# Kernel optimization log

Hardware: AMD Instinct MI355X
Metric: run time of the kernel (lower is better)

The kernel has to match this reference:

```python
import jax, jax.numpy as jnp
import numpy as np


def setup_inputs() -> dict:
    key = jax.random.key(0)
    ks = jax.random.split(key, 7)
    T, B, D, H, Q = 256, 128, 1024, 2048, 1024
    return {
        "x": jax.random.normal(ks[0], (T, B, D), dtype=jnp.float32),
        "h0": jax.random.normal(ks[1], (B, H), dtype=jnp.float32) * 0.01,
        "W_xh": jax.random.normal(ks[2], (D, H), dtype=jnp.float32) * 0.01,
        "W_hh": jax.random.normal(ks[3], (H, H), dtype=jnp.float32) * 0.01,
        "b_h": jnp.zeros((H,), dtype=jnp.float32),
        "W_hq": jax.random.normal(ks[4], (H, Q), dtype=jnp.float32) * 0.01,
        "b_q": jnp.zeros((Q,), dtype=jnp.float32),
    }


def reference(x, h0, W_xh, W_hh, b_h, W_hq, b_q):
    # x: (T, B, D); vanilla RNN recurrence with ReLU, per-step output projection.
    def step(h, xt):
        h = jax.nn.relu(xt @ W_xh + h @ W_hh + b_h)  # (B, H)
        return h, h @ W_hq + b_q                      # (B, Q)

    h, outs = jax.lax.scan(step, h0, x)               # outs: (T, B, Q)
    out = outs.reshape(-1, outs.shape[-1])            # torch.cat along dim 0 -> (T*B, Q)
    return out, h
```

## Files before the change

kernel.cpp:

```cpp
#include <hip/hip_runtime.h>
#include <hip/hip_bf16.h>

typedef __bf16 bf16_t;
typedef bf16_t bf16x8 __attribute__((ext_vector_type(8)));
typedef bf16_t bf16x4 __attribute__((ext_vector_type(4)));
typedef bf16_t bf16x2 __attribute__((ext_vector_type(2)));
typedef float f32x4 __attribute__((ext_vector_type(4)));
typedef float f32x2 __attribute__((ext_vector_type(2)));

__device__ __forceinline__ void load_lds16(const bf16_t* g, bf16_t* l) {
  __builtin_amdgcn_global_load_lds(
      (const __attribute__((address_space(1))) unsigned int*)g,
      (__attribute__((address_space(3))) unsigned int*)l,
      16, 0, 0);
}

__global__ void conv_f32_bf16(const float* __restrict__ src,
                              bf16_t* __restrict__ dst, long n) {
  long i = ((long)blockIdx.x * blockDim.x + threadIdx.x) * 8;
  if (i + 7 >= n) return;
  float4 a = *(const float4*)(src + i);
  float4 b = *(const float4*)(src + i + 4);
  bf16x8 v;
  v[0] = (bf16_t)a.x; v[1] = (bf16_t)a.y; v[2] = (bf16_t)a.z; v[3] = (bf16_t)a.w;
  v[4] = (bf16_t)b.x; v[5] = (bf16_t)b.y; v[6] = (bf16_t)b.z; v[7] = (bf16_t)b.w;
  *(bf16x8*)(dst + i) = v;
}

__global__ void conv_bf16_f32(const bf16_t* __restrict__ src,
                              float* __restrict__ dst, long n) {
  long i = (long)blockIdx.x * blockDim.x + threadIdx.x;
  if (i >= n) return;
  dst[i] = (float)src[i];
}

__global__ void transpose_conv(const float* __restrict__ src,
                               bf16_t* __restrict__ dst, int Ksrc, int Nsrc) {
  __shared__ float tile[32][33];
  int n0 = blockIdx.x * 32, k0 = blockIdx.y * 32;
  int tx = threadIdx.x, ty = threadIdx.y;
#pragma unroll
  for (int i = 0; i < 32; i += 8)
    tile[ty + i][tx] = src[(long)(k0 + ty + i) * Nsrc + n0 + tx];
  __syncthreads();
#pragma unroll
  for (int i = 0; i < 32; i += 8)
    dst[(long)(n0 + ty + i) * Ksrc + k0 + tx] = (bf16_t)tile[tx][ty + i];
}

template <int STORE_MODE>
__global__ __launch_bounds__(256) void gemm_bt_128(
    const bf16_t* __restrict__ A, const bf16_t* __restrict__ Bt,
    const float* __restrict__ bias, void* __restrict__ Dout,
    int M, int N, int K) {
  __shared__ bf16_t As[128 * 32];
  __shared__ bf16_t Bs[128 * 32];
  const int tid = threadIdx.x;
  const int lane = tid & 63;
  const int w = tid >> 6;
  const int wr = w >> 1, wc = w & 1;
  const int m0 = blockIdx.y * 128, n0 = blockIdx.x * 128;

  f32x4 acc[4][4] = {};

  const int r0 = tid >> 2;
  const int kk = (tid & 3) * 8;
  const int fr = lane & 15;
  const int fk = (lane >> 4) * 8;

  for (int k0 = 0; k0 < K; k0 += 32) {
    load_lds16(A + (long)(m0 + r0) * K + k0 + kk, As + w * 512);
    load_lds16(A + (long)(m0 + 64 + r0) * K + k0 + kk, As + 2048 + w * 512);
    load_lds16(Bt + (long)(n0 + r0) * K + k0 + kk, Bs + w * 512);
    load_lds16(Bt + (long)(n0 + 64 + r0) * K + k0 + kk, Bs + 2048 + w * 512);
    asm volatile("s_waitcnt vmcnt(0)" ::: "memory");
    __syncthreads();

    bf16x8 af[4], bfx[4];
#pragma unroll
    for (int m = 0; m < 4; ++m)
      af[m] = *(const bf16x8*)&As[(wr * 64 + m * 16 + fr) * 32 + fk];
#pragma unroll
    for (int n = 0; n < 4; ++n)
      bfx[n] = *(const bf16x8*)&Bs[(wc * 64 + n * 16 + fr) * 32 + fk];
#pragma unroll
    for (int m = 0; m < 4; ++m)
#pragma unroll
      for (int n = 0; n < 4; ++n)
        acc[m][n] = __builtin_amdgcn_mfma_f32_16x16x32_bf16(af[m], bfx[n],
                                                            acc[m][n], 0, 0, 0);
    __syncthreads();
  }

  const int fq = lane >> 4;
#pragma unroll
  for (int m = 0; m < 4; ++m) {
#pragma unroll
    for (int n = 0; n < 4; ++n) {
      int col = n0 + wc * 64 + n * 16 + fr;
      float bv = bias[col];
#pragma unroll
      for (int r = 0; r < 4; ++r) {
        int row = m0 + wr * 64 + m * 16 + fq * 4 + r;
        float v = acc[m][n][r] + bv;
        if (STORE_MODE == 0)
          ((float*)Dout)[(long)row * N + col] = v;
        else
          ((bf16_t*)Dout)[(long)row * N + col] = (bf16_t)v;
      }
    }
  }
}

__device__ __forceinline__ void half_bar(unsigned int* c, unsigned int target,
                                         int lane) {
  if (lane == 0)
    __hip_atomic_fetch_add(c, 1u, __ATOMIC_RELEASE,
                           __HIP_MEMORY_SCOPE_WORKGROUP);
  unsigned int v;
  do {
    v = __hip_atomic_load(c, __ATOMIC_ACQUIRE, __HIP_MEMORY_SCOPE_WORKGROUP);
    if (v >= target) break;
    __builtin_amdgcn_s_sleep(1);
  } while (true);
}

__global__ __launch_bounds__(512, 1) void rnn_persistent14(
    const bf16_t* __restrict__ h0,
    bf16_t* __restrict__ Hbuf,
    const bf16_t* __restrict__ WhhT,
    const bf16_t* __restrict__ WhqT,
    const float* __restrict__ bq,
    float* __restrict__ out,
    unsigned int* __restrict__ flags) {
  __shared__ bf16_t Wlds[65536];
  __shared__ float sred[2][4][16 * 36];
  __shared__ bf16_t qred[2][4][16 * 20];
  __shared__ unsigned int barc[2];
  __shared__ unsigned int sfree[2];
  __shared__ unsigned int qbc[2];
  __shared__ unsigned int qfree[2];

  const int tid = threadIdx.x, lane = tid & 63, w = tid >> 6;
  const int h = w >> 2;
  const int lw = w & 3;
  const int gid = blockIdx.x;
  const int p = (gid >> 1) & 3;
  const int n0idx = ((gid & 1) << 5) | (gid >> 3);
  const int chain = p + h * 4;
  const int m0 = chain * 16, n0 = n0idx * 32;
  const int H = 2048;
  const long BH = 128L * 2048;
  const int kb = lw * 512;
  const int fr = lane & 15, fg = lane >> 4;
  const int w64 = lw * 64;
  const int qcol0 = n0idx * 16;

  {
    const int scol = tid >> 4;
    const int sk16 = tid & 15;
    const bf16_t* gsrc = WhhT + (long)(n0 + scol) * H + sk16 * 8;
#pragma unroll 4
    for (int j = 0; j < 16; ++j) {
      bf16x8 v = *(const bf16x8*)(gsrc + j * 128);
      int k8 = sk16 + j * 16;
      *(bf16x8*)&Wlds[(k8 * 32 + scol) * 8] = v;
    }
  }
  if (tid < 2) { barc[tid] = 0; sfree[tid] = 0; qbc[tid] = 0; qfree[tid] = 0; }

  const bf16_t* Wq = WhqT + (long)(qcol0 + fr) * H + kb + fg * 8;
#define LOADPIN(dst, off)                                                     \
  bf16x8 dst = *(const bf16x8*)(Wq + (off));                                  \
  {                                                                           \
    f32x4 t_ = __builtin_bit_cast(f32x4, dst);                                \
    asm volatile("" : "+v"(t_));                                              \
    dst = __builtin_bit_cast(bf16x8, t_);                                     \
  }
  LOADPIN(q0, 0)    LOADPIN(q1, 32)   LOADPIN(q2, 64)   LOADPIN(q3, 96)
  LOADPIN(q4, 128)  LOADPIN(q5, 160)  LOADPIN(q6, 192)  LOADPIN(q7, 224)
  LOADPIN(q8, 256)  LOADPIN(q9, 288)  LOADPIN(q10, 320) LOADPIN(q11, 352)
  LOADPIN(q12, 384) LOADPIN(q13, 416) LOADPIN(q14, 448) LOADPIN(q15, 480)
#undef LOADPIN
  __syncthreads();

  if (h == 1) __builtin_amdgcn_s_sleep(64);

  const int zrowW = lane >> 2, zcolW = (lane & 3) * 8;
  const int sidx = zrowW * 36 + zcolW;
  const long zoffW = (long)(m0 + zrowW) * H + n0 + zcolW;

  const int qrow = lane >> 2, qc4 = (lane & 3) * 4;
  const f32x4 bqv = *(const f32x4*)(bq + qcol0 + qc4);

  unsigned int* myflag = flags + (((chain << 6) | n0idx) << 4);
  const unsigned int* pollflag =
      flags + (((chain << 6) | (lw * 16 + (lane & 15))) << 4);
  unsigned int* bc = &barc[h];
  unsigned int* sf = &sfree[h];
  unsigned int* qc = &qbc[h];
  unsigned int* qf = &qfree[h];

  for (int t = 0; t < 256; ++t) {
    const bf16_t* hp = (t == 0) ? h0 : Hbuf + (long)(t - 1) * BH;
    bf16_t* z = Hbuf + (long)t * BH;
    const int ew = t & 3;
    const int ew2 = (t + 2) & 3;

    f32x4 zvr;
    if (lw == ew) {
      const bf16_t* zp = z + zoffW;
      asm volatile("global_load_dwordx4 %0, %1, off sc0 sc1"
                   : "=v"(zvr)
                   : "v"(zp)
                   : "memory");
    }

    if (t > 0) {
      const unsigned int tt = (unsigned int)t;
      unsigned int v = __hip_atomic_load(pollflag, __ATOMIC_RELAXED,
                                         __HIP_MEMORY_SCOPE_AGENT);
      if (!__all(v >= tt)) {
        __builtin_amdgcn_s_sleep(1);
        v = __hip_atomic_load(pollflag, __ATOMIC_RELAXED,
                              __HIP_MEMORY_SCOPE_AGENT);
        if (!__all(v >= tt)) {
          __builtin_amdgcn_s_sleep(2);
          v = __hip_atomic_load(pollflag, __ATOMIC_RELAXED,
                                __HIP_MEMORY_SCOPE_AGENT);
          if (!__all(v >= tt)) {
            __builtin_amdgcn_s_sleep(4);
            v = __hip_atomic_load(pollflag, __ATOMIC_RELAXED,
                                  __HIP_MEMORY_SCOPE_AGENT);
            while (!__all(v >= tt)) {
              __builtin_amdgcn_s_sleep(8);
              v = __hip_atomic_load(pollflag, __ATOMIC_RELAXED,
                                    __HIP_MEMORY_SCOPE_AGENT);
            }
          }
        }
      }
    }

    const bf16_t* Ab = hp + (long)(m0 + fr) * H + kb + fg * 8;
    f32x4 a0, a1, a2, a3, a4, a5, a6, a7, a8, a9, a10, a11, a12, a13, a14, a15;
    asm volatile(
        "global_load_dwordx4 %0, %16, off sc0\n\t"
        "global_load_dwordx4 %1, %16, off offset:64 sc0\n\t"
        "global_load_dwordx4 %2, %16, off offset:128 sc0\n\t"
        "global_load_dwordx4 %3, %16, off offset:192 sc0\n\t"
        "global_load_dwordx4 %4, %16, off offset:256 sc0\n\t"
        "global_load_dwordx4 %5, %16, off offset:320 sc0\n\t"
        "global_load_dwordx4 %6, %16, off offset:384 sc0\n\t"
        "global_load_dwordx4 %7, %16, off offset:448 sc0\n\t"
        "global_load_dwordx4 %8, %16, off offset:512 sc0\n\t"
        "global_load_dwordx4 %9, %16, off offset:576 sc0\n\t"
        "global_load_dwordx4 %10, %16, off offset:640 sc0\n\t"
        "global_load_dwordx4 %11, %16, off offset:704 sc0\n\t"
        "global_load_dwordx4 %12, %16, off offset:768 sc0\n\t"
        "global_load_dwordx4 %13, %16, off offset:832 sc0\n\t"
        "global_load_dwordx4 %14, %16, off offset:896 sc0\n\t"
        "global_load_dwordx4 %15, %16, off offset:960 sc0"
        : "=&v"(a0), "=&v"(a1), "=&v"(a2), "=&v"(a3), "=&v"(a4), "=&v"(a5),
          "=&v"(a6), "=&v"(a7), "=&v"(a8), "=&v"(a9), "=&v"(a10), "=&v"(a11),
          "=&v"(a12), "=&v"(a13), "=&v"(a14), "=&v"(a15)
        : "v"(Ab)
        : "memory");

    f32x4 acc0 = {}, acc1 = {};
#define STEPX(ks, A)                                                          \
  {                                                                           \
    bf16x8 w0 = *(const bf16x8*)&Wlds[((w64 + (ks) * 4 + fg) * 32 + fr) * 8]; \
    bf16x8 w1 =                                                               \
        *(const bf16x8*)&Wlds[((w64 + (ks) * 4 + fg) * 32 + 16 + fr) * 8];    \
    bf16x8 av = __builtin_bit_cast(bf16x8, A);                                \
    acc0 = __builtin_amdgcn_mfma_f32_16x16x32_bf16(av, w0, acc0, 0, 0, 0);    \
    acc1 = __builtin_amdgcn_mfma_f32_16x16x32_bf16(av, w1, acc1, 0, 0, 0);    \
  }
    asm volatile("s_waitcnt vmcnt(8)" ::: "memory");
    __builtin_amdgcn_sched_barrier(0);
    STEPX(0, a0)   STEPX(1, a1)   STEPX(2, a2)   STEPX(3, a3)
    STEPX(4, a4)   STEPX(5, a5)   STEPX(6, a6)   STEPX(7, a7)
    asm volatile("s_waitcnt vmcnt(0)" ::: "memory");
    __builtin_amdgcn_sched_barrier(0);
    STEPX(8, a8)   STEPX(9, a9)   STEPX(10, a10) STEPX(11, a11)
    STEPX(12, a12) STEPX(13, a13) STEPX(14, a14) STEPX(15, a15)
#undef STEPX

    if (t > 0) {
      while (__hip_atomic_load(sf, __ATOMIC_ACQUIRE,
                               __HIP_MEMORY_SCOPE_WORKGROUP) <
             (unsigned int)t)
        __builtin_amdgcn_s_sleep(1);
    }

#pragma unroll
    for (int rr = 0; rr < 4; ++rr) {
      sred[h][lw][(fg * 4 + rr) * 36 + fr] = acc0[rr];
      sred[h][lw][(fg * 4 + rr) * 36 + 16 + fr] = acc1[rr];
    }
    half_bar(bc, (unsigned int)(t + 1) * 4, lane);

    if (lw == ew) {
      f32x4 slo = *(const f32x4*)&sred[h][0][sidx];
      f32x4 shi = *(const f32x4*)&sred[h][0][sidx + 4];
#pragma unroll
      for (int ww = 1; ww < 4; ++ww) {
        slo = slo + *(const f32x4*)&sred[h][ww][sidx];
        shi = shi + *(const f32x4*)&sred[h][ww][sidx + 4];
      }
      bf16x8 zv = __builtin_bit_cast(bf16x8, zvr);
      bf16x8 o;
#pragma unroll
      for (int c = 0; c < 4; ++c) {
        float v0 = slo[c] + (float)zv[c];
        float v1 = shi[c] + (float)zv[c + 4];
        o[c] = (bf16_t)(v0 > 0.f ? v0 : 0.f);
        o[c + 4] = (bf16_t)(v1 > 0.f ? v1 : 0.f);
      }
      const bf16_t* zp = z + zoffW;
      {
        f32x4 ov = __builtin_bit_cast(f32x4, o);
        asm volatile("global_store_dwordx4 %0, %1, off sc0 sc1" ::"v"(zp),
                     "v"(ov)
                     : "memory");
      }
      asm volatile("s_waitcnt vmcnt(0)" ::: "memory");
      if (lane == 0) {
        __hip_atomic_store(myflag, (unsigned int)(t + 1), __ATOMIC_RELAXED,
                           __HIP_MEMORY_SCOPE_AGENT);
        __hip_atomic_store(sf, (unsigned int)(t + 1), __ATOMIC_RELEASE,
                           __HIP_MEMORY_SCOPE_WORKGROUP);
      }
    }

    if (t > 0) {
      f32x4 qacc = {};
#define QSTEP(A, QW)                                                          \
  qacc = __builtin_amdgcn_mfma_f32_16x16x32_bf16(                             \
      __builtin_bit_cast(bf16x8, A), QW, qacc, 0, 0, 0);
      QSTEP(a0, q0)   QSTEP(a1, q1)   QSTEP(a2, q2)   QSTEP(a3, q3)
      QSTEP(a4, q4)   QSTEP(a5, q5)   QSTEP(a6, q6)   QSTEP(a7, q7)
      QSTEP(a8, q8)   QSTEP(a9, q9)   QSTEP(a10, q10) QSTEP(a11, q11)
      QSTEP(a12, q12) QSTEP(a13, q13) QSTEP(a14, q14) QSTEP(a15, q15)
#undef QSTEP
      while (__hip_atomic_load(qf, __ATOMIC_ACQUIRE,
                               __HIP_MEMORY_SCOPE_WORKGROUP) <
             (unsigned int)(t - 1))
        __builtin_amdgcn_s_sleep(1);
#pragma unroll
      for (int rr = 0; rr < 4; ++rr)
        qred[h][lw][(fg * 4 + rr) * 20 + fr] = (bf16_t)qacc[rr];
      half_bar(qc, (unsigned int)t * 4, lane);

      if (lw == ew2) {
        f32x4 s = bqv;
#pragma unroll
        for (int ww = 0; ww < 4; ++ww)
#pragma unroll
          for (int j = 0; j < 4; ++j)
            s[j] += (float)qred[h][ww][qrow * 20 + qc4 + j];
        float* op = out + ((long)(t - 1) * 128 + m0 + qrow) * 1024 + qcol0 + qc4;
        *(f32x4*)op = s;
        if (lane == 0)
          __hip_atomic_store(qf, (unsigned int)t, __ATOMIC_RELEASE,
                             __HIP_MEMORY_SCOPE_WORKGROUP);
      }
    }
  }

  {
    const unsigned int tt = 256u;
    unsigned int v;
    do {
      v = __hip_atomic_load(pollflag, __ATOMIC_RELAXED,
                            __HIP_MEMORY_SCOPE_AGENT);
      if (__all(v >= tt)) break;
      __builtin_amdgcn_s_sleep(2);
    } while (true);

    const bf16_t* hp = Hbuf + 255L * BH;
    const bf16_t* Ab = hp + (long)(m0 + fr) * H + kb + fg * 8;
    f32x4 a0, a1, a2, a3, a4, a5, a6, a7, a8, a9, a10, a11, a12, a13, a14, a15;
    asm volatile(
        "global_load_dwordx4 %0, %16, off sc0\n\t"
        "global_load_dwordx4 %1, %16, off offset:64 sc0\n\t"
        "global_load_dwordx4 %2, %16, off offset:128 sc0\n\t"
        "global_load_dwordx4 %3, %16, off offset:192 sc0\n\t"
        "global_load_dwordx4 %4, %16, off offset:256 sc0\n\t"
        "global_load_dwordx4 %5, %16, off offset:320 sc0\n\t"
        "global_load_dwordx4 %6, %16, off offset:384 sc0\n\t"
        "global_load_dwordx4 %7, %16, off offset:448 sc0\n\t"
        "global_load_dwordx4 %8, %16, off offset:512 sc0\n\t"
        "global_load_dwordx4 %9, %16, off offset:576 sc0\n\t"
        "global_load_dwordx4 %10, %16, off offset:640 sc0\n\t"
        "global_load_dwordx4 %11, %16, off offset:704 sc0\n\t"
        "global_load_dwordx4 %12, %16, off offset:768 sc0\n\t"
        "global_load_dwordx4 %13, %16, off offset:832 sc0\n\t"
        "global_load_dwordx4 %14, %16, off offset:896 sc0\n\t"
        "global_load_dwordx4 %15, %16, off offset:960 sc0\n\t"
        "s_waitcnt vmcnt(0)"
        : "=&v"(a0), "=&v"(a1), "=&v"(a2), "=&v"(a3), "=&v"(a4), "=&v"(a5),
          "=&v"(a6), "=&v"(a7), "=&v"(a8), "=&v"(a9), "=&v"(a10), "=&v"(a11),
          "=&v"(a12), "=&v"(a13), "=&v"(a14), "=&v"(a15)
        : "v"(Ab)
        : "memory");
    __builtin_amdgcn_sched_barrier(0);

    f32x4 qacc = {};
#define QSTEP(A, QW)                                                          \
  qacc = __builtin_amdgcn_mfma_f32_16x16x32_bf16(                             \
      __builtin_bit_cast(bf16x8, A), QW, qacc, 0, 0, 0);
    QSTEP(a0, q0)   QSTEP(a1, q1)   QSTEP(a2, q2)   QSTEP(a3, q3)
    QSTEP(a4, q4)   QSTEP(a5, q5)   QSTEP(a6, q6)   QSTEP(a7, q7)
    QSTEP(a8, q8)   QSTEP(a9, q9)   QSTEP(a10, q10) QSTEP(a11, q11)
    QSTEP(a12, q12) QSTEP(a13, q13) QSTEP(a14, q14) QSTEP(a15, q15)
#undef QSTEP
    while (__hip_atomic_load(qf, __ATOMIC_ACQUIRE,
                             __HIP_MEMORY_SCOPE_WORKGROUP) < 255u)
      __builtin_amdgcn_s_sleep(1);
#pragma unroll
    for (int rr = 0; rr < 4; ++rr)
      qred[h][lw][(fg * 4 + rr) * 20 + fr] = (bf16_t)qacc[rr];
    half_bar(qc, 256u * 4, lane);

    if (lw == ((256 + 2) & 3)) {
      f32x4 s = bqv;
#pragma unroll
      for (int ww = 0; ww < 4; ++ww)
#pragma unroll
        for (int j = 0; j < 4; ++j)
          s[j] += (float)qred[h][ww][qrow * 20 + qc4 + j];
      float* op = out + (255L * 128 + m0 + qrow) * 1024 + qcol0 + qc4;
      *(f32x4*)op = s;
    }
  }
}

extern "C" void kernel_launch(void* const* d_in, const int* in_sizes, int n_in,
                              void* d_out, int out_size, void* d_ws,
                              size_t ws_size, hipStream_t stream) {
  const float* x   = (const float*)d_in[0];
  const float* h0  = (const float*)d_in[1];
  const float* Wxh = (const float*)d_in[2];
  const float* Whh = (const float*)d_in[3];
  const float* bh  = (const float*)d_in[4];
  const float* Whq = (const float*)d_in[5];
  const float* bq  = (const float*)d_in[6];
  float* out = (float*)d_out;

  const int T = 256, B = 128, D = 1024, H = 2048, Q = 1024;
  const long MB = (long)T * B;

  char* ws = (char*)d_ws;
  unsigned int* flags = (unsigned int*)ws;  ws += 512 * 64;
  bf16_t* x_bf = (bf16_t*)ws;  ws += MB * D * 2;
  bf16_t* Hbuf = (bf16_t*)ws;  ws += MB * H * 2;
  bf16_t* h0bf = (bf16_t*)ws;  ws += (long)B * H * 2;
  bf16_t* WxhT = (bf16_t*)ws;  ws += (long)H * D * 2;
  bf16_t* WhhT = (bf16_t*)ws;  ws += (long)H * H * 2;
  bf16_t* WhqT = (bf16_t*)ws;  ws += (long)Q * H * 2;

  hipMemsetAsync(flags, 0, 512 * 64, stream);

  conv_f32_bf16<<<(int)(MB * D / 8 / 256), 256, 0, stream>>>(x, x_bf, MB * D);
  conv_f32_bf16<<<(int)((long)B * H / 8 / 256), 256, 0, stream>>>(h0, h0bf,
                                                                  (long)B * H);
  transpose_conv<<<dim3(H / 32, D / 32), dim3(32, 8), 0, stream>>>(Wxh, WxhT, D, H);
  transpose_conv<<<dim3(H / 32, H / 32), dim3(32, 8), 0, stream>>>(Whh, WhhT, H, H);
  transpose_conv<<<dim3(Q / 32, H / 32), dim3(32, 8), 0, stream>>>(Whq, WhqT, H, Q);

  gemm_bt_128<1><<<dim3(H / 128, MB / 128), 256, 0, stream>>>(
      x_bf, WxhT, bh, Hbuf, (int)MB, H, D);

  rnn_persistent14<<<256, 512, 0, stream>>>(h0bf, Hbuf, WhhT, WhqT, bq, out,
                                            flags);

  conv_bf16_f32<<<(int)((long)B * H / 256), 256, 0, stream>>>(
      Hbuf + (long)(T - 1) * B * H, out + MB * Q, (long)B * H);
}
```

Before: 1.564 ms.

## Fuse input projection GEMM into persistent RNN kernel with register-pinned W_xh slices

Removes the separate x@W_xh GEMM kernel and computes each step's input projection inside the persistent recurrence kernel. Each wave pins its slice of W_xh in registers, loads the x tile for the step, and runs the MFMAs before the h@W_hh part; the bias is now added in the epilogue. This eliminates a large prepass GEMM and the bf16 Hbuf round-trip of the projected input. In exchange it adds per-step global loads and MFMA work, plus extra register pressure, inside the latency-critical serial loop.

Measured after the change: 1.621 ms. +3.6%, slower.

```diff
diff --git a/kernel.cpp b/kernel.cpp
--- a/kernel.cpp
+++ b/kernel.cpp
@@ -4,7 +4,6 @@
 typedef __bf16 bf16_t;
 typedef bf16_t bf16x8 __attribute__((ext_vector_type(8)));
 typedef bf16_t bf16x4 __attribute__((ext_vector_type(4)));
-typedef bf16_t bf16x2 __attribute__((ext_vector_type(2)));
 typedef float f32x4 __attribute__((ext_vector_type(4)));
 typedef float f32x2 __attribute__((ext_vector_type(2)));
 
@@ -46,70 +45,6 @@
 #pragma unroll
   for (int i = 0; i < 32; i += 8)
     dst[(long)(n0 + ty + i) * Ksrc + k0 + tx] = (bf16_t)tile[tx][ty + i];
-}
-
-template <int STORE_MODE>
-__global__ __launch_bounds__(256) void gemm_bt_128(
-    const bf16_t* __restrict__ A, const bf16_t* __restrict__ Bt,
-    const float* __restrict__ bias, void* __restrict__ Dout,
-    int M, int N, int K) {
-  __shared__ bf16_t As[128 * 32];
-  __shared__ bf16_t Bs[128 * 32];
-  const int tid = threadIdx.x;
-  const int lane = tid & 63;
-  const int w = tid >> 6;
-  const int wr = w >> 1, wc = w & 1;
-  const int m0 = blockIdx.y * 128, n0 = blockIdx.x * 128;
-
-  f32x4 acc[4][4] = {};
-
-  const int r0 = tid >> 2;
-  const int kk = (tid & 3) * 8;
-  const int fr = lane & 15;
-  const int fk = (lane >> 4) * 8;
-
-  for (int k0 = 0; k0 < K; k0 += 32) {
-    load_lds16(A + (long)(m0 + r0) * K + k0 + kk, As + w * 512);
-    load_lds16(A + (long)(m0 + 64 + r0) * K + k0 + kk, As + 2048 + w * 512);
-    load_lds16(Bt + (long)(n0 + r0) * K + k0 + kk, Bs + w * 512);
-    load_lds16(Bt + (long)(n0 + 64 + r0) * K + k0 + kk, Bs + 2048 + w * 512);
-    asm volatile("s_waitcnt vmcnt(0)" ::: "memory");
-    __syncthreads();
-
-    bf16x8 af[4], bfx[4];
-#pragma unroll
-    for (int m = 0; m < 4; ++m)
-      af[m] = *(const bf16x8*)&As[(wr * 64 + m * 16 + fr) * 32 + fk];
-#pragma unroll
-    for (int n = 0; n < 4; ++n)
-      bfx[n] = *(const bf16x8*)&Bs[(wc * 64 + n * 16 + fr) * 32 + fk];
-#pragma unroll
-    for (int m = 0; m < 4; ++m)
-#pragma unroll
-      for (int n = 0; n < 4; ++n)
-        acc[m][n] = __builtin_amdgcn_mfma_f32_16x16x32_bf16(af[m], bfx[n],
-                                                            acc[m][n], 0, 0, 0);
-    __syncthreads();
-  }
-
-  const int fq = lane >> 4;
-#pragma unroll
-  for (int m = 0; m < 4; ++m) {
-#pragma unroll
-    for (int n = 0; n < 4; ++n) {
-      int col = n0 + wc * 64 + n * 16 + fr;
-      float bv = bias[col];
-#pragma unroll
-      for (int r = 0; r < 4; ++r) {
-        int row = m0 + wr * 64 + m * 16 + fq * 4 + r;
-        float v = acc[m][n][r] + bv;
-        if (STORE_MODE == 0)
-          ((float*)Dout)[(long)row * N + col] = v;
-        else
-          ((bf16_t*)Dout)[(long)row * N + col] = (bf16_t)v;
-      }
-    }
-  }
 }
 
 __device__ __forceinline__ void half_bar(unsigned int* c, unsigned int target,
@@ -125,10 +60,13 @@
   } while (true);
 }
 
-__global__ __launch_bounds__(512, 1) void rnn_persistent14(
+__global__ __launch_bounds__(512, 1) void rnn_persistent15(
     const bf16_t* __restrict__ h0,
+    const bf16_t* __restrict__ xb,
     bf16_t* __restrict__ Hbuf,
     const bf16_t* __restrict__ WhhT,
+    const bf16_t* __restrict__ WxhT,
+    const float* __restrict__ bh,
     const bf16_t* __restrict__ WhqT,
     const float* __restrict__ bq,
     float* __restrict__ out,
@@ -152,6 +90,7 @@
   const int H = 2048;
   const long BH = 128L * 2048;
   const int kb = lw * 512;
+  const int kbx = lw * 256;
   const int fr = lane & 15, fg = lane >> 4;
   const int w64 = lw * 64;
   const int qcol0 = n0idx * 16;
@@ -169,18 +108,28 @@
   }
   if (tid < 2) { barc[tid] = 0; sfree[tid] = 0; qbc[tid] = 0; qfree[tid] = 0; }
 
-  const bf16_t* Wq = WhqT + (long)(qcol0 + fr) * H + kb + fg * 8;
-#define LOADPIN(dst, off)                                                     \
-  bf16x8 dst = *(const bf16x8*)(Wq + (off));                                  \
+#define LOADPIN(dst, addr)                                                    \
+  bf16x8 dst = *(const bf16x8*)(addr);                                        \
   {                                                                           \
     f32x4 t_ = __builtin_bit_cast(f32x4, dst);                                \
     asm volatile("" : "+v"(t_));                                              \
     dst = __builtin_bit_cast(bf16x8, t_);                                     \
   }
-  LOADPIN(q0, 0)    LOADPIN(q1, 32)   LOADPIN(q2, 64)   LOADPIN(q3, 96)
-  LOADPIN(q4, 128)  LOADPIN(q5, 160)  LOADPIN(q6, 192)  LOADPIN(q7, 224)
-  LOADPIN(q8, 256)  LOADPIN(q9, 288)  LOADPIN(q10, 320) LOADPIN(q11, 352)
-  LOADPIN(q12, 384) LOADPIN(q13, 416) LOADPIN(q14, 448) LOADPIN(q15, 480)
+  const bf16_t* Wq = WhqT + (long)(qcol0 + fr) * H + kb + fg * 8;
+  LOADPIN(q0, Wq + 0)    LOADPIN(q1, Wq + 32)   LOADPIN(q2, Wq + 64)
+  LOADPIN(q3, Wq + 96)   LOADPIN(q4, Wq + 128)  LOADPIN(q5, Wq + 160)
+  LOADPIN(q6, Wq + 192)  LOADPIN(q7, Wq + 224)  LOADPIN(q8, Wq + 256)
+  LOADPIN(q9, Wq + 288)  LOADPIN(q10, Wq + 320) LOADPIN(q11, Wq + 352)
+  LOADPIN(q12, Wq + 384) LOADPIN(q13, Wq + 416) LOADPIN(q14, Wq + 448)
+  LOADPIN(q15, Wq + 480)
+  const bf16_t* Wx0 = WxhT + (long)(n0 + fr) * 1024 + kbx + fg * 8;
+  const bf16_t* Wx1 = WxhT + (long)(n0 + 16 + fr) * 1024 + kbx + fg * 8;
+  LOADPIN(wx0, Wx0 + 0)   LOADPIN(wx1, Wx0 + 32)  LOADPIN(wx2, Wx0 + 64)
+  LOADPIN(wx3, Wx0 + 96)  LOADPIN(wx4, Wx0 + 128) LOADPIN(wx5, Wx0 + 160)
+  LOADPIN(wx6, Wx0 + 192) LOADPIN(wx7, Wx0 + 224)
+  LOADPIN(wy0, Wx1 + 0)   LOADPIN(wy1, Wx1 + 32)  LOADPIN(wy2, Wx1 + 64)
+  LOADPIN(wy3, Wx1 + 96)  LOADPIN(wy4, Wx1 + 128) LOADPIN(wy5, Wx1 + 160)
+  LOADPIN(wy6, Wx1 + 192) LOADPIN(wy7, Wx1 + 224)
 #undef LOADPIN
   __syncthreads();
 
@@ -189,6 +138,8 @@
   const int zrowW = lane >> 2, zcolW = (lane & 3) * 8;
   const int sidx = zrowW * 36 + zcolW;
   const long zoffW = (long)(m0 + zrowW) * H + n0 + zcolW;
+  const f32x4 bhlo = *(const f32x4*)(bh + n0 + zcolW);
+  const f32x4 bhhi = *(const f32x4*)(bh + n0 + zcolW + 4);
 
   const int qrow = lane >> 2, qc4 = (lane & 3) * 4;
   const f32x4 bqv = *(const f32x4*)(bq + qcol0 + qc4);
@@ -207,14 +158,21 @@
     const int ew = t & 3;
     const int ew2 = (t + 2) & 3;
 
-    f32x4 zvr;
-    if (lw == ew) {
-      const bf16_t* zp = z + zoffW;
-      asm volatile("global_load_dwordx4 %0, %1, off sc0 sc1"
-                   : "=v"(zvr)
-                   : "v"(zp)
-                   : "memory");
-    }
+    const bf16_t* Xb = xb + ((long)t * 128 + m0 + fr) * 1024 + kbx + fg * 8;
+    f32x4 x0, x1, x2, x3, x4, x5, x6, x7;
+    asm volatile(
+        "global_load_dwordx4 %0, %8, off sc0\n\t"
+        "global_load_dwordx4 %1, %8, off offset:64 sc0\n\t"
+        "global_load_dwordx4 %2, %8, off offset:128 sc0\n\t"
+        "global_load_dwordx4 %3, %8, off offset:192 sc0\n\t"
+        "global_load_dwordx4 %4, %8, off offset:256 sc0\n\t"
+        "global_load_dwordx4 %5, %8, off offset:320 sc0\n\t"
+        "global_load_dwordx4 %6, %8, off offset:384 sc0\n\t"
+        "global_load_dwordx4 %7, %8, off offset:448 sc0"
+        : "=&v"(x0), "=&v"(x1), "=&v"(x2), "=&v"(x3), "=&v"(x4), "=&v"(x5),
+          "=&v"(x6), "=&v"(x7)
+        : "v"(Xb)
+        : "memory");
 
     if (t > 0) {
       const unsigned int tt = (unsigned int)t;
@@ -241,6 +199,20 @@
         }
       }
     }
+
+    asm volatile("s_waitcnt vmcnt(0)" ::: "memory");
+    __builtin_amdgcn_sched_barrier(0);
+    f32x4 acc0 = {}, acc1 = {};
+#define XSTEP(A, W0, W1)                                                      \
+  {                                                                           \
+    bf16x8 av = __builtin_bit_cast(bf16x8, A);                                \
+    acc0 = __builtin_amdgcn_mfma_f32_16x16x32_bf16(av, W0, acc0, 0, 0, 0);    \
+    acc1 = __builtin_amdgcn_mfma_f32_16x16x32_bf16(av, W1, acc1, 0, 0, 0);    \
+  }
+    XSTEP(x0, wx0, wy0) XSTEP(x1, wx1, wy1) XSTEP(x2, wx2, wy2)
+    XSTEP(x3, wx3, wy3) XSTEP(x4, wx4, wy4) XSTEP(x5, wx5, wy5)
+    XSTEP(x6, wx6, wy6) XSTEP(x7, wx7, wy7)
+#undef XSTEP
 
     const bf16_t* Ab = hp + (long)(m0 + fr) * H + kb + fg * 8;
     f32x4 a0, a1, a2, a3, a4, a5, a6, a7, a8, a9, a10, a11, a12, a13, a14, a15;
@@ -267,7 +239,6 @@
         : "v"(Ab)
         : "memory");
 
-    f32x4 acc0 = {}, acc1 = {};
 #define STEPX(ks, A)                                                          \
   {                                                                           \
     bf16x8 w0 = *(const bf16x8*)&Wlds[((w64 + (ks) * 4 + fg) * 32 + fr) * 8]; \
@@ -309,12 +280,11 @@
         slo = slo + *(const f32x4*)&sred[h][ww][sidx];
         shi = shi + *(const f32x4*)&sred[h][ww][sidx + 4];
       }
-      bf16x8 zv = __builtin_bit_cast(bf16x8, zvr);
       bf16x8 o;
 #pragma unroll
       for (int c = 0; c < 4; ++c) {
-        float v0 = slo[c] + (float)zv[c];
-        float v1 = shi[c] + (float)zv[c + 4];
+        float v0 = slo[c] + bhlo[c];
+        float v1 = shi[c] + bhhi[c];
         o[c] = (bf16_t)(v0 > 0.f ? v0 : 0.f);
         o[c + 4] = (bf16_t)(v1 > 0.f ? v1 : 0.f);
       }
@@ -470,11 +440,8 @@
   transpose_conv<<<dim3(H / 32, H / 32), dim3(32, 8), 0, stream>>>(Whh, WhhT, H, H);
   transpose_conv<<<dim3(Q / 32, H / 32), dim3(32, 8), 0, stream>>>(Whq, WhqT, H, Q);
 
-  gemm_bt_128<1><<<dim3(H / 128, MB / 128), 256, 0, stream>>>(
-      x_bf, WxhT, bh, Hbuf, (int)MB, H, D);
-
-  rnn_persistent14<<<256, 512, 0, stream>>>(h0bf, Hbuf, WhhT, WhqT, bq, out,
-                                            flags);
+  rnn_persistent15<<<256, 512, 0, stream>>>(h0bf, x_bf, Hbuf, WhhT, WxhT, bh,
+                                            WhqT, bq, out, flags);
 
   conv_bf16_f32<<<(int)((long)B * H / 256), 256, 0, stream>>>(
       Hbuf + (long)(T - 1) * B * H, out + MB * Q, (long)B * H);
```

## Replace per-step flag handshakes with data-embedded sign-bit validity in double-buffered hidden slots

Applied to the files above, without the earlier changes.

Drops the global flag array and its store-wait-then-flag publish. Each step's hidden state now goes into one of two ping-pong slots, with the bf16 sign bits XOR-flipped on alternating slot generations, so consumers poll the data itself. A load counts as valid when every sign bit matches the expected parity, which works because ReLU outputs are non-negative. This removes a release round trip and a separate flag poll from the serial critical path, at the cost of re-reading the full A blob on every spin and an extra XOR decode. It also relies on bf16 stores of 16 bytes never being observed torn.

Result: slower. 1.893 ms (+21.0%).

```diff
diff --git a/kernel.cpp b/kernel.cpp
--- a/kernel.cpp
+++ b/kernel.cpp
@@ -3,10 +3,8 @@
 
 typedef __bf16 bf16_t;
 typedef bf16_t bf16x8 __attribute__((ext_vector_type(8)));
-typedef bf16_t bf16x4 __attribute__((ext_vector_type(4)));
-typedef bf16_t bf16x2 __attribute__((ext_vector_type(2)));
 typedef float f32x4 __attribute__((ext_vector_type(4)));
-typedef float f32x2 __attribute__((ext_vector_type(2)));
+typedef unsigned int u32x4 __attribute__((ext_vector_type(4)));
 
 __device__ __forceinline__ void load_lds16(const bf16_t* g, bf16_t* l) {
   __builtin_amdgcn_global_load_lds(
@@ -27,11 +25,12 @@
   *(bf16x8*)(dst + i) = v;
 }
 
-__global__ void conv_bf16_f32(const bf16_t* __restrict__ src,
-                              float* __restrict__ dst, long n) {
+__global__ void conv_dec_f32(const unsigned short* __restrict__ src,
+                             float* __restrict__ dst, long n) {
   long i = (long)blockIdx.x * blockDim.x + threadIdx.x;
   if (i >= n) return;
-  dst[i] = (float)src[i];
+  unsigned int u = ((unsigned int)(src[i] ^ 0x8000u)) << 16;
+  dst[i] = __builtin_bit_cast(float, u);
 }
 
 __global__ void transpose_conv(const float* __restrict__ src,
@@ -125,14 +124,39 @@
   } while (true);
 }
 
-__global__ __launch_bounds__(512, 1) void rnn_persistent14(
+#define ABLOB(P)                                                              \
+  asm volatile(                                                               \
+      "global_load_dwordx4 %0, %16, off sc0 sc1\n\t"                          \
+      "global_load_dwordx4 %1, %16, off offset:64 sc0 sc1\n\t"                \
+      "global_load_dwordx4 %2, %16, off offset:128 sc0 sc1\n\t"               \
+      "global_load_dwordx4 %3, %16, off offset:192 sc0 sc1\n\t"               \
+      "global_load_dwordx4 %4, %16, off offset:256 sc0 sc1\n\t"               \
+      "global_load_dwordx4 %5, %16, off offset:320 sc0 sc1\n\t"               \
+      "global_load_dwordx4 %6, %16, off offset:384 sc0 sc1\n\t"               \
+      "global_load_dwordx4 %7, %16, off offset:448 sc0 sc1\n\t"               \
+      "global_load_dwordx4 %8, %16, off offset:512 sc0 sc1\n\t"               \
+      "global_load_dwordx4 %9, %16, off offset:576 sc0 sc1\n\t"               \
+      "global_load_dwordx4 %10, %16, off offset:640 sc0 sc1\n\t"              \
+      "global_load_dwordx4 %11, %16, off offset:704 sc0 sc1\n\t"              \
+      "global_load_dwordx4 %12, %16, off offset:768 sc0 sc1\n\t"              \
+      "global_load_dwordx4 %13, %16, off offset:832 sc0 sc1\n\t"              \
+      "global_load_dwordx4 %14, %16, off offset:896 sc0 sc1\n\t"              \
+      "global_load_dwordx4 %15, %16, off offset:960 sc0 sc1\n\t"              \
+      "s_waitcnt vmcnt(0)"                                                    \
+      : "=&v"(a0), "=&v"(a1), "=&v"(a2), "=&v"(a3), "=&v"(a4), "=&v"(a5),     \
+        "=&v"(a6), "=&v"(a7), "=&v"(a8), "=&v"(a9), "=&v"(a10), "=&v"(a11),   \
+        "=&v"(a12), "=&v"(a13), "=&v"(a14), "=&v"(a15)                        \
+      : "v"(P)                                                                \
+      : "memory")
+
+__global__ __launch_bounds__(512, 1) void rnn_persistent17(
     const bf16_t* __restrict__ h0,
-    bf16_t* __restrict__ Hbuf,
+    const bf16_t* __restrict__ Zbuf,
+    bf16_t* __restrict__ Hslots,
     const bf16_t* __restrict__ WhhT,
     const bf16_t* __restrict__ WhqT,
     const float* __restrict__ bq,
-    float* __restrict__ out,
-    unsigned int* __restrict__ flags) {
+    float* __restrict__ out) {
   __shared__ bf16_t Wlds[65536];
   __shared__ float sred[2][4][16 * 36];
   __shared__ bf16_t qred[2][4][16 * 20];
@@ -193,79 +217,70 @@
   const int qrow = lane >> 2, qc4 = (lane & 3) * 4;
   const f32x4 bqv = *(const f32x4*)(bq + qcol0 + qc4);
 
-  unsigned int* myflag = flags + (((chain << 6) | n0idx) << 4);
-  const unsigned int* pollflag =
-      flags + (((chain << 6) | (lw * 16 + (lane & 15))) << 4);
   unsigned int* bc = &barc[h];
   unsigned int* sf = &sfree[h];
   unsigned int* qc = &qbc[h];
   unsigned int* qf = &qfree[h];
 
+  const long aoff = (long)(m0 + fr) * H + kb + fg * 8;
+
   for (int t = 0; t < 256; ++t) {
-    const bf16_t* hp = (t == 0) ? h0 : Hbuf + (long)(t - 1) * BH;
-    bf16_t* z = Hbuf + (long)t * BH;
+    const bf16_t* z = Zbuf + (long)t * BH;
     const int ew = t & 3;
     const int ew2 = (t + 2) & 3;
 
-    f32x4 zvr;
-    if (lw == ew) {
-      const bf16_t* zp = z + zoffW;
-      asm volatile("global_load_dwordx4 %0, %1, off sc0 sc1"
-                   : "=v"(zvr)
-                   : "v"(zp)
-                   : "memory");
-    }
-
-    if (t > 0) {
-      const unsigned int tt = (unsigned int)t;
-      unsigned int v = __hip_atomic_load(pollflag, __ATOMIC_RELAXED,
-                                         __HIP_MEMORY_SCOPE_AGENT);
-      if (!__all(v >= tt)) {
-        __builtin_amdgcn_s_sleep(1);
-        v = __hip_atomic_load(pollflag, __ATOMIC_RELAXED,
-                              __HIP_MEMORY_SCOPE_AGENT);
-        if (!__all(v >= tt)) {
-          __builtin_amdgcn_s_sleep(2);
-          v = __hip_atomic_load(pollflag, __ATOMIC_RELAXED,
-                                __HIP_MEMORY_SCOPE_AGENT);
-          if (!__all(v >= tt)) {
-            __builtin_amdgcn_s_sleep(4);
-            v = __hip_atomic_load(pollflag, __ATOMIC_RELAXED,
-                                  __HIP_MEMORY_SCOPE_AGENT);
-            while (!__all(v >= tt)) {
-              __builtin_amdgcn_s_sleep(8);
-              v = __hip_atomic_load(pollflag, __ATOMIC_RELAXED,
-                                    __HIP_MEMORY_SCOPE_AGENT);
-            }
-          }
+    f32x4 zvr = {};
+    if (lw == ew) zvr = *(const f32x4*)(z + zoffW);
+
+    f32x4 a0, a1, a2, a3, a4, a5, a6, a7, a8, a9, a10, a11, a12, a13, a14, a15;
+    if (t == 0) {
+      const bf16_t* Ab = h0 + aoff;
+      ABLOB(Ab);
+      __builtin_amdgcn_sched_barrier(0);
+    } else {
+      const bf16_t* Ab = Hslots + ((long)((t - 1) & 1)) * BH + aoff;
+      const unsigned int expect =
+          (((t - 1) >> 1) & 1) ? 0x80008000u : 0u;
+      for (;;) {
+        ABLOB(Ab);
+        __builtin_amdgcn_sched_barrier(0);
+        bool rdy;
+        if (expect) {
+          u32x4 m = __builtin_bit_cast(u32x4, a0);
+          m &= __builtin_bit_cast(u32x4, a1);  m &= __builtin_bit_cast(u32x4, a2);
+          m &= __builtin_bit_cast(u32x4, a3);  m &= __builtin_bit_cast(u32x4, a4);
+          m &= __builtin_bit_cast(u32x4, a5);  m &= __builtin_bit_cast(u32x4, a6);
+          m &= __builtin_bit_cast(u32x4, a7);  m &= __builtin_bit_cast(u32x4, a8);
+          m &= __builtin_bit_cast(u32x4, a9);  m &= __builtin_bit_cast(u32x4, a10);
+          m &= __builtin_bit_cast(u32x4, a11); m &= __builtin_bit_cast(u32x4, a12);
+          m &= __builtin_bit_cast(u32x4, a13); m &= __builtin_bit_cast(u32x4, a14);
+          m &= __builtin_bit_cast(u32x4, a15);
+          unsigned int c = m[0] & m[1] & m[2] & m[3];
+          rdy = ((~c) & 0x80008000u) == 0u;
+        } else {
+          u32x4 m = __builtin_bit_cast(u32x4, a0);
+          m |= __builtin_bit_cast(u32x4, a1);  m |= __builtin_bit_cast(u32x4, a2);
+          m |= __builtin_bit_cast(u32x4, a3);  m |= __builtin_bit_cast(u32x4, a4);
+          m |= __builtin_bit_cast(u32x4, a5);  m |= __builtin_bit_cast(u32x4, a6);
+          m |= __builtin_bit_cast(u32x4, a7);  m |= __builtin_bit_cast(u32x4, a8);
+          m |= __builtin_bit_cast(u32x4, a9);  m |= __builtin_bit_cast(u32x4, a10);
+          m |= __builtin_bit_cast(u32x4, a11); m |= __builtin_bit_cast(u32x4, a12);
+          m |= __builtin_bit_cast(u32x4, a13); m |= __builtin_bit_cast(u32x4, a14);
+          m |= __builtin_bit_cast(u32x4, a15);
+          unsigned int c = m[0] | m[1] | m[2] | m[3];
+          rdy = (c & 0x80008000u) == 0u;
         }
-      }
-    }
-
-    const bf16_t* Ab = hp + (long)(m0 + fr) * H + kb + fg * 8;
-    f32x4 a0, a1, a2, a3, a4, a5, a6, a7, a8, a9, a10, a11, a12, a13, a14, a15;
-    asm volatile(
-        "global_load_dwordx4 %0, %16, off sc0\n\t"
-        "global_load_dwordx4 %1, %16, off offset:64 sc0\n\t"
-        "global_load_dwordx4 %2, %16, off offset:128 sc0\n\t"
-        "global_load_dwordx4 %3, %16, off offset:192 sc0\n\t"
-        "global_load_dwordx4 %4, %16, off offset:256 sc0\n\t"
-        "global_load_dwordx4 %5, %16, off offset:320 sc0\n\t"
-        "global_load_dwordx4 %6, %16, off offset:384 sc0\n\t"
-        "global_load_dwordx4 %7, %16, off offset:448 sc0\n\t"
-        "global_load_dwordx4 %8, %16, off offset:512 sc0\n\t"
-        "global_load_dwordx4 %9, %16, off offset:576 sc0\n\t"
-        "global_load_dwordx4 %10, %16, off offset:640 sc0\n\t"
-        "global_load_dwordx4 %11, %16, off offset:704 sc0\n\t"
-        "global_load_dwordx4 %12, %16, off offset:768 sc0\n\t"
-        "global_load_dwordx4 %13, %16, off offset:832 sc0\n\t"
-        "global_load_dwordx4 %14, %16, off offset:896 sc0\n\t"
-        "global_load_dwordx4 %15, %16, off offset:960 sc0"
-        : "=&v"(a0), "=&v"(a1), "=&v"(a2), "=&v"(a3), "=&v"(a4), "=&v"(a5),
-          "=&v"(a6), "=&v"(a7), "=&v"(a8), "=&v"(a9), "=&v"(a10), "=&v"(a11),
-          "=&v"(a12), "=&v"(a13), "=&v"(a14), "=&v"(a15)
-        : "v"(Ab)
-        : "memory");
+        if (__all(rdy)) break;
+        __builtin_amdgcn_s_sleep(2);
+      }
+      if (expect) {
+        const u32x4 msk = {0x80008000u, 0x80008000u, 0x80008000u, 0x80008000u};
+#define DEC(A) A = __builtin_bit_cast(f32x4, __builtin_bit_cast(u32x4, A) ^ msk);
+        DEC(a0) DEC(a1) DEC(a2) DEC(a3) DEC(a4) DEC(a5) DEC(a6) DEC(a7)
+        DEC(a8) DEC(a9) DEC(a10) DEC(a11) DEC(a12) DEC(a13) DEC(a14) DEC(a15)
+#undef DEC
+      }
+    }
 
     f32x4 acc0 = {}, acc1 = {};
 #define STEPX(ks, A)                                                          \
@@ -277,12 +292,8 @@
     acc0 = __builtin_amdgcn_mfma_f32_16x16x32_bf16(av, w0, acc0, 0, 0, 0);    \
     acc1 = __builtin_amdgcn_mfma_f32_16x16x32_bf16(av, w1, acc1, 0, 0, 0);    \
   }
-    asm volatile("s_waitcnt vmcnt(8)" ::: "memory");
-    __builtin_amdgcn_sched_barrier(0);
     STEPX(0, a0)   STEPX(1, a1)   STEPX(2, a2)   STEPX(3, a3)
     STEPX(4, a4)   STEPX(5, a5)   STEPX(6, a6)   STEPX(7, a7)
-    asm volatile("s_waitcnt vmcnt(0)" ::: "memory");
-    __builtin_amdgcn_sched_barrier(0);
     STEPX(8, a8)   STEPX(9, a9)   STEPX(10, a10) STEPX(11, a11)
     STEPX(12, a12) STEPX(13, a13) STEPX(14, a14) STEPX(15, a15)
 #undef STEPX
@@ -318,20 +329,21 @@
         o[c] = (bf16_t)(v0 > 0.f ? v0 : 0.f);
         o[c + 4] = (bf16_t)(v1 > 0.f ? v1 : 0.f);
       }
-      const bf16_t* zp = z + zoffW;
+      u32x4 ov = __builtin_bit_cast(u32x4, o);
+      if ((t >> 1) & 1) {
+        const u32x4 msk = {0x80008000u, 0x80008000u, 0x80008000u, 0x80008000u};
+        ov ^= msk;
+      }
+      bf16_t* hp = Hslots + ((long)(t & 1)) * BH + zoffW;
       {
-        f32x4 ov = __builtin_bit_cast(f32x4, o);
-        asm volatile("global_store_dwordx4 %0, %1, off sc0 sc1" ::"v"(zp),
-                     "v"(ov)
+        f32x4 of = __builtin_bit_cast(f32x4, ov);
+        asm volatile("global_store_dwordx4 %0, %1, off sc0 sc1" ::"v"(hp),
+                     "v"(of)
                      : "memory");
       }
-      asm volatile("s_waitcnt vmcnt(0)" ::: "memory");
-      if (lane == 0) {
-        __hip_atomic_store(myflag, (unsigned int)(t + 1), __ATOMIC_RELAXED,
-                           __HIP_MEMORY_SCOPE_AGENT);
+      if (lane == 0)
         __hip_atomic_store(sf, (unsigned int)(t + 1), __ATOMIC_RELEASE,
                            __HIP_MEMORY_SCOPE_WORKGROUP);
-      }
     }
 
     if (t > 0) {
@@ -370,42 +382,31 @@
   }
 
   {
-    const unsigned int tt = 256u;
-    unsigned int v;
-    do {
-      v = __hip_atomic_load(pollflag, __ATOMIC_RELAXED,
-                            __HIP_MEMORY_SCOPE_AGENT);
-      if (__all(v >= tt)) break;
+    const bf16_t* Ab = Hslots + BH + aoff;
+    f32x4 a0, a1, a2, a3, a4, a5, a6, a7, a8, a9, a10, a11, a12, a13, a14, a15;
+    for (;;) {
+      ABLOB(Ab);
+      __builtin_amdgcn_sched_barrier(0);
+      u32x4 m = __builtin_bit_cast(u32x4, a0);
+      m &= __builtin_bit_cast(u32x4, a1);  m &= __builtin_bit_cast(u32x4, a2);
+      m &= __builtin_bit_cast(u32x4, a3);  m &= __builtin_bit_cast(u32x4, a4);
+      m &= __builtin_bit_cast(u32x4, a5);  m &= __builtin_bit_cast(u32x4, a6);
+      m &= __builtin_bit_cast(u32x4, a7);  m &= __builtin_bit_cast(u32x4, a8);
+      m &= __builtin_bit_cast(u32x4, a9);  m &= __builtin_bit_cast(u32x4, a10);
+      m &= __builtin_bit_cast(u32x4, a11); m &= __builtin_bit_cast(u32x4, a12);
+      m &= __builtin_bit_cast(u32x4, a13); m &= __builtin_bit_cast(u32x4, a14);
+      m &= __builtin_bit_cast(u32x4, a15);
+      unsigned int c = m[0] & m[1] & m[2] & m[3];
+      if (__all(((~c) & 0x80008000u) == 0u)) break;
       __builtin_amdgcn_s_sleep(2);
-    } while (true);
-
-    const bf16_t* hp = Hbuf + 255L * BH;
-    const bf16_t* Ab = hp + (long)(m0 + fr) * H + kb + fg * 8;
-    f32x4 a0, a1, a2, a3, a4, a5, a6, a7, a8, a9, a10, a11, a12, a13, a14, a15;
-    asm volatile(
-        "global_load_dwordx4 %0, %16, off sc0\n\t"
-        "global_load_dwordx4 %1, %16, off offset:64 sc0\n\t"
-        "global_load_dwordx4 %2, %16, off offset:128 sc0\n\t"
-        "global_load_dwordx4 %3, %16, off offset:192 sc0\n\t"
-        "global_load_dwordx4 %4, %16, off offset:256 sc0\n\t"
-        "global_load_dwordx4 %5, %16, off offset:320 sc0\n\t"
-        "global_load_dwordx4 %6, %16, off offset:384 sc0\n\t"
-        "global_load_dwordx4 %7, %16, off offset:448 sc0\n\t"
-        "global_load_dwordx4 %8, %16, off offset:512 sc0\n\t"
-        "global_load_dwordx4 %9, %16, off offset:576 sc0\n\t"
-        "global_load_dwordx4 %10, %16, off offset:640 sc0\n\t"
-        "global_load_dwordx4 %11, %16, off offset:704 sc0\n\t"
-        "global_load_dwordx4 %12, %16, off offset:768 sc0\n\t"
-        "global_load_dwordx4 %13, %16, off offset:832 sc0\n\t"
-        "global_load_dwordx4 %14, %16, off offset:896 sc0\n\t"
-        "global_load_dwordx4 %15, %16, off offset:960 sc0\n\t"
-        "s_waitcnt vmcnt(0)"
-        : "=&v"(a0), "=&v"(a1), "=&v"(a2), "=&v"(a3), "=&v"(a4), "=&v"(a5),
-          "=&v"(a6), "=&v"(a7), "=&v"(a8), "=&v"(a9), "=&v"(a10), "=&v"(a11),
-          "=&v"(a12), "=&v"(a13), "=&v"(a14), "=&v"(a15)
-        : "v"(Ab)
-        : "memory");
-    __builtin_amdgcn_sched_barrier(0);
+    }
+    {
+      const u32x4 msk = {0x80008000u, 0x80008000u, 0x80008000u, 0x80008000u};
+#define DEC(A) A = __builtin_bit_cast(f32x4, __builtin_bit_cast(u32x4, A) ^ msk);
+      DEC(a0) DEC(a1) DEC(a2) DEC(a3) DEC(a4) DEC(a5) DEC(a6) DEC(a7)
+      DEC(a8) DEC(a9) DEC(a10) DEC(a11) DEC(a12) DEC(a13) DEC(a14) DEC(a15)
+#undef DEC
+    }
 
     f32x4 qacc = {};
 #define QSTEP(A, QW)                                                          \
@@ -436,6 +437,7 @@
     }
   }
 }
+#undef ABLOB
 
 extern "C" void kernel_launch(void* const* d_in, const int* in_sizes, int n_in,
                               void* d_out, int out_size, void* d_ws,
@@ -453,15 +455,15 @@
   const long MB = (long)T * B;
 
   char* ws = (char*)d_ws;
-  unsigned int* flags = (unsigned int*)ws;  ws += 512 * 64;
+  bf16_t* Hslots = (bf16_t*)ws;  ws += 2L * B * H * 2;
   bf16_t* x_bf = (bf16_t*)ws;  ws += MB * D * 2;
-  bf16_t* Hbuf = (bf16_t*)ws;  ws += MB * H * 2;
+  bf16_t* Zbuf = (bf16_t*)ws;  ws += MB * H * 2;
   bf16_t* h0bf = (bf16_t*)ws;  ws += (long)B * H * 2;
   bf16_t* WxhT = (bf16_t*)ws;  ws += (long)H * D * 2;
   bf16_t* WhhT = (bf16_t*)ws;  ws += (long)H * H * 2;
   bf16_t* WhqT = (bf16_t*)ws;  ws += (long)Q * H * 2;
 
-  hipMemsetAsync(flags, 0, 512 * 64, stream);
+  hipMemsetAsync(Hslots, 0xAA, 2L * B * H * 2, stream);
 
   conv_f32_bf16<<<(int)(MB * D / 8 / 256), 256, 0, stream>>>(x, x_bf, MB * D);
   conv_f32_bf16<<<(int)((long)B * H / 8 / 256), 256, 0, stream>>>(h0, h0bf,
@@ -471,11 +473,12 @@
   transpose_conv<<<dim3(Q / 32, H / 32), dim3(32, 8), 0, stream>>>(Whq, WhqT, H, Q);
 
   gemm_bt_128<1><<<dim3(H / 128, MB / 128), 256, 0, stream>>>(
-      x_bf, WxhT, bh, Hbuf, (int)MB, H, D);
-
-  rnn_persistent14<<<256, 512, 0, stream>>>(h0bf, Hbuf, WhhT, WhqT, bq, out,
-                                            flags);
-
-  conv_bf16_f32<<<(int)((long)B * H / 256), 256, 0, stream>>>(
-      Hbuf + (long)(T - 1) * B * H, out + MB * Q, (long)B * H);
-}
+      x_bf, WxhT, bh, Zbuf, (int)MB, H, D);
+
+  rnn_persistent17<<<256, 512, 0, stream>>>(h0bf, Zbuf, Hslots, WhhT, WhqT,
+                                            bq, out);
+
+  conv_dec_f32<<<(int)((long)B * H / 256), 256, 0, stream>>>(
+      (const unsigned short*)(Hslots + (long)B * H), out + MB * Q,
+      (long)B * H);
+}
```
